# Kernel optimization log

Measured on AMD Instinct MI355X. Metric: run time of the kernel, lower is better.

## Reference

```python
import jax, jax.numpy as jnp
import numpy as np

B, S, H, A = 16, 2048, 1024, 1024


def setup_inputs() -> dict:
    key = jax.random.key(0)
    k1, k2, k3 = jax.random.split(key, 3)
    x = jax.random.normal(k1, (B, S, H), dtype=jnp.float32)
    # learned params (nn.Parameter tensors in the torch module)
    w_a = jax.random.normal(k2, (H, A), dtype=jnp.float32) * 0.02
    query = jax.random.normal(k3, (H, A), dtype=jnp.float32) * 0.02
    return {"x": x, "w_a": w_a, "query": query}


def reference(x, w_a, query):
    # semantic attention: values = x
    key = jnp.tanh(x @ w_a)          # [B, S, A]
    q = x @ query                    # [B, S, A]  (per-token semantic query)
    # temp[b, s, t] = q[b, s] . key[b, t]
    temp = jnp.einsum('bsa,bta->bst', q, key)  # [B, S, S]
    seq_len = x.shape[1]
    # softmax mask: strictly-upper triangle = -inf, lower+diag = 0 (causal)
    causal = jnp.triu(jnp.ones((seq_len, seq_len), dtype=bool), k=1)
    softmax_mask = jnp.where(causal, -jnp.inf, 0.0).astype(x.dtype)
    d = jax.nn.softmax(temp + softmax_mask, axis=-1)  # [B, S, S]
    a = d @ x                        # [B, S, H]
    return (a, d)
```

## Files before the change

### kernel.cpp

```cpp
#include <hip/hip_runtime.h>

typedef _Float16 f16x8 __attribute__((ext_vector_type(8)));
typedef float f32x4 __attribute__((ext_vector_type(4)));
typedef unsigned short u16;
typedef u16 u16x4 __attribute__((ext_vector_type(4)));
typedef u16 u16x8 __attribute__((ext_vector_type(8)));

#define NBATCH 16
#define NSEQ   2048
#define NHID   1024
#define MALL   (NBATCH * NSEQ)

__device__ __forceinline__ u16 f16_rne(float x) {
    _Float16 h = (_Float16)x;
    return __builtin_bit_cast(u16, h);
}
__device__ __forceinline__ float fast_tanh(float x) {
    float e = __expf(2.0f * x);
    return 1.0f - 2.0f / (e + 1.0f);
}

#define GLOAD16(g, l) __builtin_amdgcn_global_load_lds(                         \
    (const __attribute__((address_space(1))) unsigned int*)(g),                 \
    (__attribute__((address_space(3))) unsigned int*)(l), 16, 0, 0)


#define NOPS ((void)0)
#define VMW4 asm volatile("s_waitcnt vmcnt(4)" ::: "memory");
#define VMW0 asm volatile("s_waitcnt vmcnt(0)" ::: "memory");

#define MMQ(MH, I, J0, J1, J2, J3)                                             \
    MM(acc[MH][0][(I)&3][0], I, J0); MM(acc[MH][0][(I)&3][1], I, J1);          \
    MM(acc[MH][1][(I)&3][0], I, J2); MM(acc[MH][1][(I)&3][1], I, J3);

#define MMBLK_P(MH)                                                            \
    MMQ(MH,0,0,1,2,3) MMQ(MH,1,0,1,2,3) MMQ(MH,2,0,1,2,3) MMQ(MH,3,0,1,2,3)    \
    MMQ(MH,4,4,5,6,7) MMQ(MH,5,4,5,6,7) MMQ(MH,6,4,5,6,7) MMQ(MH,7,4,5,6,7)

#define TILE64(C, ST0, ST1, W) {                                               \
    LDA(0,C,0,0); LDA(1,C,0,0); LDA(2,C,0,0); LDA(3,C,0,0);                    \
    LDA(4,C,0,1); LDA(5,C,0,1); LDA(6,C,0,1); LDA(7,C,0,1);                    \
    LDB(0,C,0,0); LDB(1,C,0,0); LDB(2,C,1,0); LDB(3,C,1,0);                    \
    LDB(4,C,0,1); LDB(5,C,0,1); LDB(6,C,1,1); LDB(7,C,1,1);                    \
    ST0;                                                                       \
    __builtin_amdgcn_s_barrier();                                              \
    asm volatile("s_waitcnt lgkmcnt(0)" ::: "memory");                         \
    __builtin_amdgcn_sched_barrier(0);                                         \
    __builtin_amdgcn_s_setprio(1);                                             \
    MMBLK_P(0)                                                                 \
    __builtin_amdgcn_s_setprio(0);                                             \
    __builtin_amdgcn_s_barrier();                                              \
    LDA(0,C,1,0); LDA(1,C,1,0); LDA(2,C,1,0); LDA(3,C,1,0);                    \
    LDA(4,C,1,1); LDA(5,C,1,1); LDA(6,C,1,1); LDA(7,C,1,1);                    \
    ST1;                                                                       \
    __builtin_amdgcn_s_barrier();                                              \
    asm volatile("s_waitcnt lgkmcnt(0)" ::: "memory");                         \
    __builtin_amdgcn_sched_barrier(0);                                         \
    __builtin_amdgcn_s_setprio(1);                                             \
    MMBLK_P(1)                                                                 \
    __builtin_amdgcn_s_setprio(0);                                             \
    W;                                                                         \
    __builtin_amdgcn_s_barrier();                                              \
}

__device__ __forceinline__ void gemm_core64(
    const u16* __restrict__ Ap, int Arow0,
    const u16* __restrict__ Bp, int Brow0,
    u16* lds, f32x4 (&acc)[2][2][4][2])
{
    int tid = threadIdx.x;
    int l = tid & 63, w = tid >> 6;
    int wr = w >> 2, wc = w & 3;
    int fr = l & 15, sg = l >> 4;

    f16x8 ah[8], bh[8];

    auto LDA = [&](int i, int C, int MH, int KH) {
        int rb = MH * 128 + wr * 64 + (i & 3) * 16 + fr;
        int sl = ((KH * 4 + sg) ^ (rb & 7)) * 8;
        ah[i] = *(const f16x8*)&lds[C * 32768 + rb * 64 + sl];
    };
    auto LDB = [&](int j, int C, int NH, int KH) {
        int rb = NH * 128 + wc * 32 + (j & 1) * 16 + fr;
        int sl = ((KH * 4 + sg) ^ (rb & 7)) * 8;
        bh[j] = *(const f16x8*)&lds[C * 32768 + 16384 + rb * 64 + sl];
    };
    auto MM = [&](f32x4& d, int i, int j) {
        d = __builtin_amdgcn_mfma_f32_16x16x32_f16(ah[i], bh[j], d, 0, 0, 0);
    };
    auto STA = [&](int C, int H, int T) {
        int rg = Arow0 + H * 128 + w * 8 + (l >> 3);
        const u16* s = Ap + (size_t)rg * 1024 + (size_t)T * 64
                       + ((l & 7) ^ (rg & 7)) * 8;
        u16* d = &lds[C * 32768 + (H * 128 + w * 8) * 64];
        GLOAD16(s, d);
        GLOAD16(s + (size_t)64 * 1024, d + 64 * 64);
    };
    auto STB = [&](int C, int H, int T) {
        int rg = Brow0 + H * 128 + w * 8 + (l >> 3);
        const u16* s = Bp + (size_t)rg * 1024 + (size_t)T * 64
                       + ((l & 7) ^ (rg & 7)) * 8;
        u16* d = &lds[C * 32768 + 16384 + (H * 128 + w * 8) * 64];
        GLOAD16(s, d);
        GLOAD16(s + (size_t)64 * 1024, d + 64 * 64);
    };

    STA(0, 0, 0); STA(0, 1, 0); STB(0, 0, 0); STB(0, 1, 0);
    STA(1, 0, 1); STB(1, 0, 1);
    VMW4
    __builtin_amdgcn_s_barrier();

    for (int u = 0; u < 13; u += 2) {
        TILE64(0, (STA(1,1,u+1), STB(1,1,u+1)), (STA(0,0,u+2), STB(0,0,u+2)), VMW4)
        TILE64(1, (STA(0,1,u+2), STB(0,1,u+2)), (STA(1,0,u+3), STB(1,0,u+3)), VMW4)
    }
    TILE64(0, (STA(1,1,15), STB(1,1,15)), NOPS, VMW0)
    TILE64(1, NOPS, NOPS, NOPS)
}

__global__ __launch_bounds__(256) void wprep_kernel(
    const float* __restrict__ wa, const float* __restrict__ qu,
    u16* __restrict__ wT)
{
    int idx = blockIdx.x * 256 + threadIdx.x;
    int h = idx >> 10, n = idx & 1023;
    wT[(size_t)n * 1024 + h]          = f16_rne(wa[idx] * 64.0f);
    wT[(size_t)(1024 + n) * 1024 + h] = f16_rne(qu[idx] * 64.0f);
}

__global__ __launch_bounds__(256) void xprep_kernel(
    const float* __restrict__ x, u16* __restrict__ xT,
    u16* __restrict__ x_f16)
{
    __shared__ u16 tile[64][68];
    int b = blockIdx.z;
    int t0 = blockIdx.x * 64;
    int h0 = blockIdx.y * 64;
    const float* xb = x + ((size_t)b * NSEQ + t0) * NHID + h0;
    int tid = threadIdx.x;
    int tl = tid >> 4;
    int hl = (tid & 15) * 4;
    #pragma unroll
    for (int i = 0; i < 4; i++) {
        int r = i * 16 + tl;
        float4 v = *(const float4*)&xb[(size_t)r * NHID + hl];
        u16x4 hv;
        hv[0] = f16_rne(v.x); hv[1] = f16_rne(v.y);
        hv[2] = f16_rne(v.z); hv[3] = f16_rne(v.w);
        *(u16x4*)&tile[r][hl] = hv;
        *(u16x4*)&x_f16[((size_t)(b * NSEQ) + t0 + r) * NHID + h0 + hl] = hv;
    }
    __syncthreads();
    u16* xTb = xT + ((size_t)b * NHID + h0) * NSEQ + t0;
    int hl2 = tid >> 4;
    int tl2 = (tid & 15) * 4;
    #pragma unroll
    for (int i = 0; i < 4; i++) {
        int hh = i * 16 + hl2;
        u16x4 o;
        o[0] = tile[tl2 + 0][hh]; o[1] = tile[tl2 + 1][hh];
        o[2] = tile[tl2 + 2][hh]; o[3] = tile[tl2 + 3][hh];
        *(u16x4*)&xTb[(size_t)hh * NSEQ + tl2] = o;
    }
}

__global__ __launch_bounds__(512, 2) void k1_gemm(
    const u16* __restrict__ x_f16, const u16* __restrict__ wT,
    u16* __restrict__ k_f16, u16* __restrict__ q_f16)
{
    extern __shared__ u16 lds[];
    int wg = blockIdx.x;
    int nid = (wg & 7) * 128 + (wg >> 3);
    int n0 = (nid & 7) * 256;
    int m0 = (nid >> 3) * 256;
    bool is_key = (n0 < 1024);

    f32x4 acc[2][2][4][2] = {};
    gemm_core64(x_f16, m0, wT, n0, lds, acc);

    int tid = threadIdx.x;
    int l = tid & 63, w = tid >> 6;
    int wr = w >> 2, wc = w & 3;
    int fr = l & 15, fq = l >> 4;
    int nb = is_key ? n0 : (n0 - 1024);
    u16* outp = is_key ? k_f16 : q_f16;
    #pragma unroll
    for (int mh = 0; mh < 2; mh++)
    #pragma unroll
    for (int nh = 0; nh < 2; nh++)
    #pragma unroll
    for (int m = 0; m < 4; m++)
    #pragma unroll
    for (int n = 0; n < 2; n++)
    #pragma unroll
    for (int j = 0; j < 4; j++) {
        int grow = m0 + mh * 128 + wr * 64 + m * 16 + fq * 4 + j;
        int c    = nb + nh * 128 + wc * 32 + n * 16 + fr;
        float v = acc[mh][nh][m][n][j] * 0.015625f;
        outp[(size_t)grow * 1024 + c] = f16_rne(is_key ? fast_tanh(v) : v);
    }
}

__global__ __launch_bounds__(512, 2) void k2_logits(
    const u16* __restrict__ q_f16, const u16* __restrict__ k_f16,
    float* __restrict__ dmat)
{
    extern __shared__ u16 lds[];
    int wg = blockIdx.x;
    int nid = (wg & 7) * 72 + (wg >> 3);
    int b = nid / 36;
    int lin = nid - b * 36;
    int st = 0;
    while ((st + 1) * (st + 2) / 2 <= lin) st++;
    int tt = lin - st * (st + 1) / 2;
    int s0 = st * 256, t0 = tt * 256;
    int base = b * NSEQ;

    f32x4 acc[2][2][4][2] = {};
    gemm_core64(q_f16, base + s0, k_f16, base + t0, lds, acc);

    float* db = dmat + (size_t)b * NSEQ * NSEQ;
    int tid = threadIdx.x;
    int l = tid & 63, w = tid >> 6;
    int wr = w >> 2, wc = w & 3;
    int fr = l & 15, fq = l >> 4;
    #pragma unroll
    for (int mh = 0; mh < 2; mh++)
    #pragma unroll
    for (int nh = 0; nh < 2; nh++)
    #pragma unroll
    for (int m = 0; m < 4; m++)
    #pragma unroll
    for (int n = 0; n < 2; n++)
    #pragma unroll
    for (int j = 0; j < 4; j++) {
        int s = s0 + mh * 128 + wr * 64 + m * 16 + fq * 4 + j;
        int t = t0 + nh * 128 + wc * 32 + n * 16 + fr;
        if (t <= s) db[(size_t)s * NSEQ + t] = acc[mh][nh][m][n][j];
    }
}

__global__ __launch_bounds__(256) void k3_softmax(
    float* __restrict__ dmat, u16* __restrict__ d_f16)
{
    __shared__ float redm[4];
    __shared__ float reds[4];
    int rowid = blockIdx.x;
    int s = rowid & (NSEQ - 1);
    float* row = dmat + (size_t)rowid * NSEQ;
    int tid = threadIdx.x;
    int lane = tid & 63, w = tid >> 6;
    int t0 = tid * 8;

    float v[8];
    if (t0 <= s) {
        float4 a = *(const float4*)&row[t0];
        float4 c = *(const float4*)&row[t0 + 4];
        v[0] = a.x; v[1] = a.y; v[2] = a.z; v[3] = a.w;
        v[4] = c.x; v[5] = c.y; v[6] = c.z; v[7] = c.w;
        #pragma unroll
        for (int i = 0; i < 8; i++) if (t0 + i > s) v[i] = -INFINITY;
    } else {
        #pragma unroll
        for (int i = 0; i < 8; i++) v[i] = -INFINITY;
    }

    float m = -INFINITY;
    #pragma unroll
    for (int i = 0; i < 8; i++) m = fmaxf(m, v[i]);
    #pragma unroll
    for (int off = 32; off > 0; off >>= 1) m = fmaxf(m, __shfl_xor(m, off));
    if (lane == 0) redm[w] = m;
    __syncthreads();
    m = fmaxf(fmaxf(redm[0], redm[1]), fmaxf(redm[2], redm[3]));

    float sum = 0.f;
    float ev[8];
    #pragma unroll
    for (int i = 0; i < 8; i++) {
        ev[i] = (t0 + i <= s) ? __expf(v[i] - m) : 0.f;
        sum += ev[i];
    }
    #pragma unroll
    for (int off = 32; off > 0; off >>= 1) sum += __shfl_xor(sum, off);
    if (lane == 0) reds[w] = sum;
    __syncthreads();
    sum = reds[0] + reds[1] + reds[2] + reds[3];
    float inv = 1.0f / sum;

    float4 o0, o1;
    o0.x = ev[0] * inv; o0.y = ev[1] * inv; o0.z = ev[2] * inv; o0.w = ev[3] * inv;
    o1.x = ev[4] * inv; o1.y = ev[5] * inv; o1.z = ev[6] * inv; o1.w = ev[7] * inv;
    *(float4*)&row[t0] = o0;
    *(float4*)&row[t0 + 4] = o1;
    u16x8 bv;
    bv[0] = f16_rne(o0.x); bv[1] = f16_rne(o0.y); bv[2] = f16_rne(o0.z); bv[3] = f16_rne(o0.w);
    bv[4] = f16_rne(o1.x); bv[5] = f16_rne(o1.y); bv[6] = f16_rne(o1.z); bv[7] = f16_rne(o1.w);
    *(u16x8*)&d_f16[(size_t)rowid * NSEQ + t0] = bv;
}

__global__ __launch_bounds__(256) void k4_av(
    const u16* __restrict__ d_f16,
    const u16* __restrict__ xT,
    float* __restrict__ aout)
{
    __shared__ u16 sa[128 * 32];
    __shared__ u16 sb[128 * 32];

    int wg = blockIdx.x;
    int nid = (wg & 7) * 256 + (wg >> 3);
    int n0 = (nid & 7) * 128;
    int s0 = ((nid >> 3) & 15) * 128;
    int b = nid >> 7;

    int tid = threadIdx.x;
    int lane = tid & 63;
    int w = tid >> 6;
    int wr = w >> 1, wc = w & 1;

    int srow = w * 16 + (lane >> 2);
    int sslot = ((lane & 3) ^ ((lane >> 3) & 3)) * 8;

    const u16* pa = d_f16 + (size_t)(b * NSEQ + s0 + srow) * NSEQ + sslot;
    const u16* pb = xT + ((size_t)b * NHID + n0 + srow) * NSEQ + sslot;
    u16* da0 = &sa[(w * 16) * 32];  u16* da1 = &sa[(64 + w * 16) * 32];
    u16* db0 = &sb[(w * 16) * 32];  u16* db1 = &sb[(64 + w * 16) * 32];
    const size_t R64 = (size_t)64 * NSEQ;

    int fr = lane & 15, sg = lane >> 4;
    int rsl = (sg ^ ((fr >> 1) & 3)) * 8;

    f32x4 acc[4][4] = {};
    int kmax = s0 + 128;

    for (int kk = 0; kk < kmax; kk += 32) {
        __syncthreads();
        GLOAD16(pa + kk, da0); GLOAD16(pa + kk + R64, da1);
        GLOAD16(pb + kk, db0); GLOAD16(pb + kk + R64, db1);
        __syncthreads();

        f16x8 af[4], bf[4];
        #pragma unroll
        for (int m = 0; m < 4; m++)
            af[m] = *(const f16x8*)&sa[(wr * 64 + m * 16 + fr) * 32 + rsl];
        #pragma unroll
        for (int n = 0; n < 4; n++)
            bf[n] = *(const f16x8*)&sb[(wc * 64 + n * 16 + fr) * 32 + rsl];
        #pragma unroll
        for (int m = 0; m < 4; m++)
            #pragma unroll
            for (int n = 0; n < 4; n++)
                acc[m][n] = __builtin_amdgcn_mfma_f32_16x16x32_f16(af[m], bf[n], acc[m][n], 0, 0, 0);
    }

    float* ab = aout + (size_t)b * NSEQ * NHID;
    int fq = lane >> 4;
    #pragma unroll
    for (int m = 0; m < 4; m++)
        #pragma unroll
        for (int n = 0; n < 4; n++)
            #pragma unroll
            for (int j = 0; j < 4; j++) {
                int s = s0 + wr * 64 + m * 16 + fq * 4 + j;
                int h = n0 + wc * 64 + n * 16 + fr;
                ab[(size_t)s * NHID + h] = acc[m][n][j];
            }
}

extern "C" void kernel_launch(void* const* d_in, const int* in_sizes, int n_in,
                              void* d_out, int out_size, void* d_ws, size_t ws_size,
                              hipStream_t stream)
{
    const float* x     = (const float*)d_in[0];
    const float* w_a   = (const float*)d_in[1];
    const float* query = (const float*)d_in[2];

    float* aout = (float*)d_out;
    float* dmat = aout + (size_t)NBATCH * NSEQ * NHID;

    char* p = (char*)d_ws;
    u16* q_f16  = (u16*)p; p += (size_t)MALL * 1024 * 2;
    u16* x_f16  = (u16*)p; p += (size_t)MALL * 1024 * 2;
    u16* k_f16  = (u16*)p; p += (size_t)MALL * 1024 * 2;
    u16* d_f16  = x_f16;
    u16* xT     = (u16*)p; p += (size_t)MALL * 1024 * 2;
    u16* wT     = (u16*)p; p += (size_t)2048 * 1024 * 2;
    (void)ws_size; (void)in_sizes; (void)n_in; (void)out_size;

    hipFuncSetAttribute((const void*)k1_gemm,
                        hipFuncAttributeMaxDynamicSharedMemorySize, 131072);
    hipFuncSetAttribute((const void*)k2_logits,
                        hipFuncAttributeMaxDynamicSharedMemorySize, 131072);

    wprep_kernel<<<dim3(4096), 256, 0, stream>>>(w_a, query, wT);
    xprep_kernel<<<dim3(32, 16, 16), 256, 0, stream>>>(x, xT, x_f16);
    k1_gemm<<<dim3(1024), 512, 131072, stream>>>(x_f16, wT, k_f16, q_f16);
    k2_logits<<<dim3(576), 512, 131072, stream>>>(q_f16, k_f16, dmat);
    k3_softmax<<<dim3(32768), 256, 0, stream>>>(dmat, d_f16);
    k4_av<<<dim3(2048), 256, 0, stream>>>(d_f16, xT, aout);
}
```

Measured before the change: 564.6 us.

## Split GEMM tile into four phases and skip masked fp16 softmax stores

Restructures the 64-wide K tile of the projection GEMM into four MFMA phases instead of two, interleaving LDS B-fragment reads and global-to-LDS async stores across more barrier-separated phases to overlap memory with compute more finely. Separately, the softmax kernel now only writes fp16 probabilities up to the end of the diagonal 128-block, skipping stores of zeros that the AV kernel presumably never reads. It adds more barriers per tile, and the skipped stores are only safe if k4_av never reads beyond the causal block. A dead macro define/undef was also added.

Measured after the change: 550.3 us. -2.5%, faster.

```diff
diff --git a/kernel.cpp b/kernel.cpp
--- a/kernel.cpp
+++ b/kernel.cpp
@@ -20,6 +20,8 @@
     return 1.0f - 2.0f / (e + 1.0f);
 }
 
+#define GLOAD16(g, l) __builtin_amdgcn_global_lds(0)
+#undef GLOAD16
 #define GLOAD16(g, l) __builtin_amdgcn_global_load_lds(                         \
     (const __attribute__((address_space(1))) unsigned int*)(g),                 \
     (__attribute__((address_space(3))) unsigned int*)(l), 16, 0, 0)
@@ -29,36 +31,47 @@
 #define VMW4 asm volatile("s_waitcnt vmcnt(4)" ::: "memory");
 #define VMW0 asm volatile("s_waitcnt vmcnt(0)" ::: "memory");
 
-#define MMQ(MH, I, J0, J1, J2, J3)                                             \
-    MM(acc[MH][0][(I)&3][0], I, J0); MM(acc[MH][0][(I)&3][1], I, J1);          \
-    MM(acc[MH][1][(I)&3][0], I, J2); MM(acc[MH][1][(I)&3][1], I, J3);
-
-#define MMBLK_P(MH)                                                            \
-    MMQ(MH,0,0,1,2,3) MMQ(MH,1,0,1,2,3) MMQ(MH,2,0,1,2,3) MMQ(MH,3,0,1,2,3)    \
-    MMQ(MH,4,4,5,6,7) MMQ(MH,5,4,5,6,7) MMQ(MH,6,4,5,6,7) MMQ(MH,7,4,5,6,7)
-
-#define TILE64(C, ST0, ST1, W) {                                               \
+#define MMPH(MH, NH)                                                           \
+    MM(acc[MH][NH][0][0], 0, (NH)*2+0); MM(acc[MH][NH][0][1], 0, (NH)*2+1);    \
+    MM(acc[MH][NH][1][0], 1, (NH)*2+0); MM(acc[MH][NH][1][1], 1, (NH)*2+1);    \
+    MM(acc[MH][NH][2][0], 2, (NH)*2+0); MM(acc[MH][NH][2][1], 2, (NH)*2+1);    \
+    MM(acc[MH][NH][3][0], 3, (NH)*2+0); MM(acc[MH][NH][3][1], 3, (NH)*2+1);    \
+    MM(acc[MH][NH][0][0], 4, (NH)*2+4); MM(acc[MH][NH][0][1], 4, (NH)*2+5);    \
+    MM(acc[MH][NH][1][0], 5, (NH)*2+4); MM(acc[MH][NH][1][1], 5, (NH)*2+5);    \
+    MM(acc[MH][NH][2][0], 6, (NH)*2+4); MM(acc[MH][NH][2][1], 6, (NH)*2+5);    \
+    MM(acc[MH][NH][3][0], 7, (NH)*2+4); MM(acc[MH][NH][3][1], 7, (NH)*2+5);
+
+#define PH_SYNC                                                                \
+    __builtin_amdgcn_s_barrier();                                              \
+    asm volatile("s_waitcnt lgkmcnt(0)" ::: "memory");                         \
+    __builtin_amdgcn_sched_barrier(0);
+
+#define TILE8(C, S1, S2, S3, S4, W) {                                          \
+                                                                \
     LDA(0,C,0,0); LDA(1,C,0,0); LDA(2,C,0,0); LDA(3,C,0,0);                    \
     LDA(4,C,0,1); LDA(5,C,0,1); LDA(6,C,0,1); LDA(7,C,0,1);                    \
-    LDB(0,C,0,0); LDB(1,C,0,0); LDB(2,C,1,0); LDB(3,C,1,0);                    \
-    LDB(4,C,0,1); LDB(5,C,0,1); LDB(6,C,1,1); LDB(7,C,1,1);                    \
-    ST0;                                                                       \
+    LDB(0,C,0,0); LDB(1,C,0,0); LDB(4,C,0,1); LDB(5,C,0,1);                    \
+    S1;                                                                        \
+    PH_SYNC                                                                    \
+    __builtin_amdgcn_s_setprio(1); MMPH(0,0) __builtin_amdgcn_s_setprio(0);    \
     __builtin_amdgcn_s_barrier();                                              \
-    asm volatile("s_waitcnt lgkmcnt(0)" ::: "memory");                         \
-    __builtin_amdgcn_sched_barrier(0);                                         \
-    __builtin_amdgcn_s_setprio(1);                                             \
-    MMBLK_P(0)                                                                 \
-    __builtin_amdgcn_s_setprio(0);                                             \
+                                                                \
+    LDB(2,C,1,0); LDB(3,C,1,0); LDB(6,C,1,1); LDB(7,C,1,1);                    \
+    S2;                                                                        \
+    PH_SYNC                                                                    \
+    __builtin_amdgcn_s_setprio(1); MMPH(0,1) __builtin_amdgcn_s_setprio(0);    \
     __builtin_amdgcn_s_barrier();                                              \
+                                                                \
     LDA(0,C,1,0); LDA(1,C,1,0); LDA(2,C,1,0); LDA(3,C,1,0);                    \
     LDA(4,C,1,1); LDA(5,C,1,1); LDA(6,C,1,1); LDA(7,C,1,1);                    \
-    ST1;                                                                       \
+    S3;                                                                        \
+    PH_SYNC                                                                    \
+    __builtin_amdgcn_s_setprio(1); MMPH(1,0) __builtin_amdgcn_s_setprio(0);    \
     __builtin_amdgcn_s_barrier();                                              \
-    asm volatile("s_waitcnt lgkmcnt(0)" ::: "memory");                         \
-    __builtin_amdgcn_sched_barrier(0);                                         \
-    __builtin_amdgcn_s_setprio(1);                                             \
-    MMBLK_P(1)                                                                 \
-    __builtin_amdgcn_s_setprio(0);                                             \
+                                                                \
+    S4;                                                                        \
+    PH_SYNC                                                                    \
+    __builtin_amdgcn_s_setprio(1); MMPH(1,1) __builtin_amdgcn_s_setprio(0);    \
     W;                                                                         \
     __builtin_amdgcn_s_barrier();                                              \
 }
@@ -111,11 +124,11 @@
     __builtin_amdgcn_s_barrier();
 
     for (int u = 0; u < 13; u += 2) {
-        TILE64(0, (STA(1,1,u+1), STB(1,1,u+1)), (STA(0,0,u+2), STB(0,0,u+2)), VMW4)
-        TILE64(1, (STA(0,1,u+2), STB(0,1,u+2)), (STA(1,0,u+3), STB(1,0,u+3)), VMW4)
-    }
-    TILE64(0, (STA(1,1,15), STB(1,1,15)), NOPS, VMW0)
-    TILE64(1, NOPS, NOPS, NOPS)
+        TILE8(0, STA(1,1,u+1), STB(1,1,u+1), STA(0,0,u+2), STB(0,0,u+2), VMW4)
+        TILE8(1, STA(0,1,u+2), STB(0,1,u+2), STA(1,0,u+3), STB(1,0,u+3), VMW4)
+    }
+    TILE8(0, STA(1,1,15), STB(1,1,15), NOPS, NOPS, VMW0)
+    TILE8(1, NOPS, NOPS, NOPS, NOPS, NOPS)
 }
 
 __global__ __launch_bounds__(256) void wprep_kernel(
@@ -293,10 +306,12 @@
     o1.x = ev[4] * inv; o1.y = ev[5] * inv; o1.z = ev[6] * inv; o1.w = ev[7] * inv;
     *(float4*)&row[t0] = o0;
     *(float4*)&row[t0 + 4] = o1;
-    u16x8 bv;
-    bv[0] = f16_rne(o0.x); bv[1] = f16_rne(o0.y); bv[2] = f16_rne(o0.z); bv[3] = f16_rne(o0.w);
-    bv[4] = f16_rne(o1.x); bv[5] = f16_rne(o1.y); bv[6] = f16_rne(o1.z); bv[7] = f16_rne(o1.w);
-    *(u16x8*)&d_f16[(size_t)rowid * NSEQ + t0] = bv;
+    if (t0 <= ((s >> 7) << 7) + 127) {
+        u16x8 bv;
+        bv[0] = f16_rne(o0.x); bv[1] = f16_rne(o0.y); bv[2] = f16_rne(o0.z); bv[3] = f16_rne(o0.w);
+        bv[4] = f16_rne(o1.x); bv[5] = f16_rne(o1.y); bv[6] = f16_rne(o1.z); bv[7] = f16_rne(o1.w);
+        *(u16x8*)&d_f16[(size_t)rowid * NSEQ + t0] = bv;
+    }
 }
 
 __global__ __launch_bounds__(256) void k4_av(
```
